# Optimization experiments

Hardware: AMD Instinct MI355X
Metric: run time of the kernel (lower is better)

The kernel has to match this reference:

```python
import jax, jax.numpy as jnp
import numpy as np

BN_EPS = 1e-3  # keras BatchNormalization default epsilon

def _prelu(x, a):
    return jnp.maximum(x, 0) + a * jnp.minimum(x, 0)

def _bn(x, g, b, m, v):
    # inference-mode batchnorm with moving statistics
    return (x - m) * jax.lax.rsqrt(v + BN_EPS) * g + b

def setup_inputs() -> dict:
    key = jax.random.key(0)
    ks = jax.random.split(key, 24)
    B, D, V, L = 4096, 768, 200000, 200000
    F = 3 * D  # 2304 = qid|pos|neg concat
    n = lambda i, shape, s=0.05: jax.random.normal(ks[i], shape, jnp.float32) * s
    return dict(
        qid_embeddings=jax.random.normal(ks[0], (B, D), jnp.float32),
        node_embeddings=n(1, (V, D), 0.1),
        leaf_embeddings=n(2, (L, D), 0.1),
        positives=jax.random.randint(ks[3], (B,), 0, V),
        negetives=jax.random.randint(ks[4], (B,), 0, V),
        p_isleafs=jax.random.randint(ks[5], (B,), 0, 2),
        n_isleafs=jax.random.randint(ks[6], (B,), 0, 2),
        W00=n(7, (F, 36)), b00=jnp.zeros((36,)), a00=jnp.full((36,), 0.25),
        W01=n(8, (36, 1)), b01=jnp.zeros((1,)),
        W1=n(9, (F, 128)), b1=jnp.zeros((128,)), a1=jnp.full((128,), 0.25),
        g1=jnp.ones((128,)), be1=n(10, (128,), 0.1), m1=n(11, (128,), 0.1),
        v1=jax.random.uniform(ks[12], (128,)) + 0.5,
        W2=n(13, (128, 64)), b2=jnp.zeros((64,)), a2=jnp.full((64,), 0.25),
        g2=jnp.ones((64,)), be2=n(14, (64,), 0.1), m2=n(15, (64,), 0.1),
        v2=jax.random.uniform(ks[16], (64,)) + 0.5,
        W3=n(17, (64, 24)), b3=jnp.zeros((24,)), a3=jnp.full((24,), 0.25),
        g3=jnp.ones((24,)), be3=n(18, (24,), 0.1), m3=n(19, (24,), 0.1),
        v3=jax.random.uniform(ks[20], (24,)) + 0.5,
        W4=n(21, (24, 2)), b4=jnp.zeros((2,)),
    )

def reference(qid_embeddings, node_embeddings, leaf_embeddings, positives, negetives,
              p_isleafs, n_isleafs, W00, b00, a00, W01, b01,
              W1, b1, a1, g1, be1, m1, v1,
              W2, b2, a2, g2, be2, m2, v2,
              W3, b3, a3, g3, be3, m3, v3, W4, b4):
    # per-sample conditional embedding gather (leaf table vs internal node table)
    pos = jnp.where((p_isleafs == 1)[:, None], leaf_embeddings[positives], node_embeddings[positives])  # [B,D]
    neg = jnp.where((n_isleafs == 1)[:, None], leaf_embeddings[negetives], node_embeddings[negetives])  # [B,D]
    q = qid_embeddings  # [B,D]
    # attention block: small Dense(36)->Dense(1) scalar weight per sample
    feat = jnp.concatenate([q, pos, neg], axis=1)  # [B,3D]
    h = _prelu(feat @ W00 + b00, a00)              # [B,36]
    w = h @ W01 + b01                              # [B,1]
    item = jnp.concatenate([w * pos, w * neg, q], axis=1)  # [B,3D]
    # MLP 2304 -> 128 -> 64 -> 24 -> 2 (layer10/20/30 unused in original call)
    x = _bn(_prelu(item @ W1 + b1, a1), g1, be1, m1, v1)
    x = _bn(_prelu(x @ W2 + b2, a2), g2, be2, m2, v2)
    x = _bn(_prelu(x @ W3 + b3, a3), g3, be3, m3, v3)
    return jax.nn.softmax(x @ W4 + b4, axis=-1)  # [B,2]
```

## Files before the change

kernel.cpp:

```cpp
#include <hip/hip_runtime.h>
#include <hip/hip_bf16.h>

typedef _Float16 half8 __attribute__((ext_vector_type(8)));
typedef _Float16 half4v __attribute__((ext_vector_type(4)));
typedef float f32x4 __attribute__((ext_vector_type(4)));

#define NCOLS 176
#define TILE_ELEMS (NCOLS*32)
#define TILE_U16 (TILE_ELEMS/8)
#define WTSTR 40
#define XSTR2 2312

#define OFF_A36 0
#define OFF_TQ  2560
#define OFF_TPN 10752
#define OFF_WV  18944
#define OFF_X1  19008
#define OFF_W2  27456
#define OFF_X2  43840
#define OFF_W3  48192
#define OFF_X3  51264
#define OFF_SCR 53056
#define SM_BYTES 77632

struct Params {
  const float *qid, *node, *leaf;
  const int *pos_idx, *neg_idx, *p_leaf, *n_leaf;
  const float *b00, *a00, *W01, *b01;
  const float *b1, *a1, *g1, *be1, *m1, *v1;
  const float *W2, *b2, *a2, *g2, *be2, *m2, *v2;
  const float *W3, *b3, *a3, *g3, *be3, *m3, *v3;
  const float *W4, *b4;
  const _Float16 *Wp;
  float *out;
};

__global__ __launch_bounds__(256) void pack_weights(const float* __restrict__ W00,
                                                    const float* __restrict__ W1,
                                                    _Float16* __restrict__ Wp) {
  int g = blockIdx.x;
  int s = g / 24, t = g - s * 24;
  int k0 = t * 32;
  int w1row0 = (s == 0) ? 1536 : (s == 1 ? 0 : 768);
  __shared__ _Float16 T[NCOLS][WTSTR];
  int tid = threadIdx.x;
  for (int u = tid; u < 1024; u += 256) {
    int kk = u >> 5, c4 = u & 31;
    float4 f = *(const float4*)(W1 + (size_t)(w1row0 + k0 + kk) * 128 + c4 * 4);
    int c = 48 + c4 * 4;
    T[c + 0][kk] = (_Float16)f.x; T[c + 1][kk] = (_Float16)f.y;
    T[c + 2][kk] = (_Float16)f.z; T[c + 3][kk] = (_Float16)f.w;
  }
  for (int u = tid; u < 1152; u += 256) {
    int kk = u / 36, c = u - kk * 36;
    T[c][kk] = (_Float16)W00[(size_t)(s * 768 + k0 + kk) * 36 + c];
  }
  for (int u = tid; u < 384; u += 256) {
    int kk = u & 31, c = 36 + (u >> 5);
    T[c][kk] = (_Float16)0.f;
  }
  __syncthreads();
  uint4* dst = (uint4*)(Wp + (size_t)g * TILE_ELEMS);
  for (int u = tid; u < TILE_U16; u += 256) {
    int c = u >> 2, q = u & 3;
    dst[u] = *(const uint4*)&T[c][q * 8];
  }
}

__global__ __launch_bounds__(512) void fused_main(Params p) {
  __shared__ __align__(16) char sm[SM_BYTES];
  __shared__ const float* Xbase[3][16];

  _Float16* X   = (_Float16*)sm;
  float*    A36 = (float*)(sm + OFF_A36);
  float*    Tq  = (float*)(sm + OFF_TQ);
  float*    Tpn = (float*)(sm + OFF_TPN);
  float*    wv  = (float*)(sm + OFF_WV);
  float*    x1  = (float*)(sm + OFF_X1);
  _Float16* W2h = (_Float16*)(sm + OFF_W2);
  float*    x2  = (float*)(sm + OFF_X2);
  _Float16* W3h = (_Float16*)(sm + OFF_W3);
  float*    x3  = (float*)(sm + OFF_X3);
  float*    scr = (float*)(sm + OFF_SCR);

  const int tid  = threadIdx.x;
  const int wid  = tid >> 6;
  const int lane = tid & 63;
  const int lm   = lane & 15;
  const int hk   = lane >> 4;
  const int nw   = wid & 3;
  const int kg   = wid >> 2;
  const int m0   = blockIdx.x * 16;
  const bool HAS2 = (nw < 3);

  if (tid < 48) {
    int s = tid >> 4, i = tid & 15;
    const float* base;
    if (s == 0) base = p.qid + (size_t)(m0 + i) * 768;
    else if (s == 1) {
      int idx = p.pos_idx[m0 + i];
      base = ((p.p_leaf[m0 + i] == 1) ? p.leaf : p.node) + (size_t)idx * 768;
    } else {
      int idx = p.neg_idx[m0 + i];
      base = ((p.n_leaf[m0 + i] == 1) ? p.leaf : p.node) + (size_t)idx * 768;
    }
    Xbase[s][i] = base;
  }
  __syncthreads();

#pragma unroll
  for (int j = 0; j < 18; ++j) {
    int v = tid + j * 512;
    int i = v / 192, c4 = v - i * 192;
    int s = i >> 4, r = i & 15;
    float4 f = ((const float4*)Xbase[s][i & 15])[c4];
    half4v h = { (_Float16)f.x, (_Float16)f.y, (_Float16)f.z, (_Float16)f.w };
    *(half4v*)(X + r * XSTR2 + s * 768 + c4 * 4) = h;
  }
  __syncthreads();

  const uint4* Wp4 = (const uint4*)p.Wp;
  const int woff = ((nw * 48 + lm) << 2) + hk;

  f32x4 accA[3] = {{0.f,0.f,0.f,0.f},{0.f,0.f,0.f,0.f},{0.f,0.f,0.f,0.f}};
  f32x4 accB[3] = {{0.f,0.f,0.f,0.f},{0.f,0.f,0.f,0.f},{0.f,0.f,0.f,0.f}};

  auto ldW = [&](int g, uint4& r0, uint4& r1, uint4& r2) {
    const uint4* b = Wp4 + (size_t)g * TILE_U16 + woff;
    r0 = b[0]; r1 = b[64];
    if (HAS2) r2 = b[128];
  };
  auto ldA = [&](int g) -> half8 {
    return *(const half8*)(X + lm * XSTR2 + g * 32 + hk * 8);
  };
  auto comp = [&](int g, uint4 w0, uint4 w1, uint4 w2, half8 a) {
    half8 b0 = __builtin_bit_cast(half8, w0);
    half8 b1 = __builtin_bit_cast(half8, w1);
    half8 b2 = __builtin_bit_cast(half8, w2);
    if ((nw == 0) || (g < 24)) {
      accA[0] = __builtin_amdgcn_mfma_f32_16x16x32_f16(a, b0, accA[0], 0, 0, 0);
      accA[1] = __builtin_amdgcn_mfma_f32_16x16x32_f16(a, b1, accA[1], 0, 0, 0);
      if (HAS2) accA[2] = __builtin_amdgcn_mfma_f32_16x16x32_f16(a, b2, accA[2], 0, 0, 0);
    } else {
      accB[0] = __builtin_amdgcn_mfma_f32_16x16x32_f16(a, b0, accB[0], 0, 0, 0);
      accB[1] = __builtin_amdgcn_mfma_f32_16x16x32_f16(a, b1, accB[1], 0, 0, 0);
      if (HAS2) accB[2] = __builtin_amdgcn_mfma_f32_16x16x32_f16(a, b2, accB[2], 0, 0, 0);
    }
  };

  uint4 A0{}, A1{}, A2{}, B0{}, B1{}, B2{};
  half8 aA, aB;
  ldW(kg, A0, A1, A2);     aA = ldA(kg);
  ldW(kg + 2, B0, B1, B2); aB = ldA(kg + 2);
#pragma unroll
  for (int t = 0; t < 36; t += 2) {
    int ga = kg + 2 * t;
    comp(ga, A0, A1, A2, aA);
    if (t + 2 < 36) { ldW(ga + 4, A0, A1, A2); aA = ldA(ga + 4); }
    comp(ga + 2, B0, B1, B2, aB);
    if (t + 3 < 36) { ldW(ga + 6, B0, B1, B2); aB = ldA(ga + 6); }
  }

  __syncthreads();
  if (kg == 1) {
#pragma unroll
    for (int n = 0; n < 3; ++n) {
      if (n < 2 || HAS2) {
#pragma unroll
        for (int r = 0; r < 4; ++r) {
          int base = ((nw * 3 + n) * 2) * 256 + (hk * 4 + r) * 16 + lm;
          scr[base]       = accA[n][r];
          scr[base + 256] = accB[n][r];
        }
      }
    }
  }
  __syncthreads();
  if (kg == 0) {
#pragma unroll
    for (int n = 0; n < 3; ++n) {
      if (n < 2 || HAS2) {
#pragma unroll
        for (int r = 0; r < 4; ++r) {
          int base = ((nw * 3 + n) * 2) * 256 + (hk * 4 + r) * 16 + lm;
          float va = accA[n][r] + scr[base];
          float vb = accB[n][r] + scr[base + 256];
          int row = hk * 4 + r;
          int col = nw * 48 + n * 16 + lm;
          if (nw == 0) { if (col < 36) A36[row * 40 + col] = va; }
          else { int rc = col - 48; Tq[row * 128 + rc] = va; Tpn[row * 128 + rc] = vb; }
        }
      }
    }
  }
  __syncthreads();

#pragma unroll
  for (int j = 0; j < 4; ++j) {
    int u = tid + j * 512;
    float4 f = ((const float4*)p.W2)[u];
    half4v h = { (_Float16)f.x, (_Float16)f.y, (_Float16)f.z, (_Float16)f.w };
    *(half4v*)(W2h + (u >> 4) * 64 + (u & 15) * 4) = h;
  }
  if (tid < 16) {
    float acc = p.b01[0];
    for (int c = 0; c < 36; ++c) {
      float h = A36[tid * 40 + c] + p.b00[c];
      h = (h > 0.f) ? h : p.a00[c] * h;
      acc += h * p.W01[c];
    }
    wv[tid] = acc;
  }
  __syncthreads();

#pragma unroll
  for (int j = 0; j < 4; ++j) {
    int u = tid + j * 512;
    int i = u >> 7, c = u & 127;
    float v = wv[i] * Tpn[i * 128 + c] + Tq[i * 128 + c] + p.b1[c];
    v = (v > 0.f) ? v : p.a1[c] * v;
    v = (v - p.m1[c]) * (1.f / sqrtf(p.v1[c] + 1e-3f)) * p.g1[c] + p.be1[c];
    x1[i * 132 + c] = v;
  }
  __syncthreads();

  if (tid < 256) {
    int i = tid & 15, cq = tid >> 4;
    const float* xr = x1 + i * 132;
    f32x4 acc0 = { p.b2[cq*4+0], p.b2[cq*4+1], p.b2[cq*4+2], p.b2[cq*4+3] };
    f32x4 acc1 = { 0.f, 0.f, 0.f, 0.f };
#pragma unroll 8
    for (int k = 0; k < 128; k += 2) {
      half4v w0 = *(const half4v*)(W2h + k * 64 + cq * 4);
      half4v w1 = *(const half4v*)(W2h + (k + 1) * 64 + cq * 4);
      acc0 += xr[k]     * __builtin_convertvector(w0, f32x4);
      acc1 += xr[k + 1] * __builtin_convertvector(w1, f32x4);
    }
    f32x4 acc = acc0 + acc1;
#pragma unroll
    for (int jj = 0; jj < 4; ++jj) {
      int c = cq * 4 + jj;
      float v = acc[jj];
      v = (v > 0.f) ? v : p.a2[c] * v;
      v = (v - p.m2[c]) * (1.f / sqrtf(p.v2[c] + 1e-3f)) * p.g2[c] + p.be2[c];
      x2[i * 68 + c] = v;
    }
  }
#pragma unroll
  for (int j = 0; j < 3; ++j) {
    int u = tid + j * 512;
    W3h[u] = (_Float16)p.W3[u];
  }
  __syncthreads();

  if (tid < 384) {
    int i = tid & 15, c = tid >> 4;
    float acc = p.b3[c];
#pragma unroll 8
    for (int k = 0; k < 64; ++k) acc += x2[i * 68 + k] * (float)W3h[k * 24 + c];
    acc = (acc > 0.f) ? acc : p.a3[c] * acc;
    acc = (acc - p.m3[c]) * (1.f / sqrtf(p.v3[c] + 1e-3f)) * p.g3[c] + p.be3[c];
    x3[i * 28 + c] = acc;
  }
  __syncthreads();

  if (tid < 16) {
    float l0 = p.b4[0], l1 = p.b4[1];
#pragma unroll
    for (int k = 0; k < 24; ++k) {
      float v = x3[tid * 28 + k];
      l0 += v * p.W4[k * 2 + 0];
      l1 += v * p.W4[k * 2 + 1];
    }
    float m = fmaxf(l0, l1);
    float e0 = __expf(l0 - m), e1 = __expf(l1 - m);
    float inv = 1.f / (e0 + e1);
    p.out[(size_t)(m0 + tid) * 2 + 0] = e0 * inv;
    p.out[(size_t)(m0 + tid) * 2 + 1] = e1 * inv;
  }
}

extern "C" void kernel_launch(void* const* d_in, const int* in_sizes, int n_in,
                              void* d_out, int out_size, void* d_ws, size_t ws_size,
                              hipStream_t stream) {
  const float* qid  = (const float*)d_in[0];
  const float* node = (const float*)d_in[1];
  const float* leaf = (const float*)d_in[2];
  const int* positives = (const int*)d_in[3];
  const int* negetives = (const int*)d_in[4];
  const int* p_isleafs = (const int*)d_in[5];
  const int* n_isleafs = (const int*)d_in[6];
  const float* W00 = (const float*)d_in[7];
  const float* b00 = (const float*)d_in[8];
  const float* a00 = (const float*)d_in[9];
  const float* W01 = (const float*)d_in[10];
  const float* b01 = (const float*)d_in[11];
  const float* W1  = (const float*)d_in[12];
  const float* b1  = (const float*)d_in[13];
  const float* a1  = (const float*)d_in[14];
  const float* g1  = (const float*)d_in[15];
  const float* be1 = (const float*)d_in[16];
  const float* m1  = (const float*)d_in[17];
  const float* v1  = (const float*)d_in[18];
  const float* W2  = (const float*)d_in[19];
  const float* b2  = (const float*)d_in[20];
  const float* a2  = (const float*)d_in[21];
  const float* g2  = (const float*)d_in[22];
  const float* be2 = (const float*)d_in[23];
  const float* m2  = (const float*)d_in[24];
  const float* v2  = (const float*)d_in[25];
  const float* W3  = (const float*)d_in[26];
  const float* b3  = (const float*)d_in[27];
  const float* a3  = (const float*)d_in[28];
  const float* g3  = (const float*)d_in[29];
  const float* be3 = (const float*)d_in[30];
  const float* m3  = (const float*)d_in[31];
  const float* v3  = (const float*)d_in[32];
  const float* W4  = (const float*)d_in[33];
  const float* b4  = (const float*)d_in[34];

  _Float16* Wp = (_Float16*)d_ws;

  pack_weights<<<72, 256, 0, stream>>>(W00, W1, Wp);

  Params p;
  p.qid = qid; p.node = node; p.leaf = leaf;
  p.pos_idx = positives; p.neg_idx = negetives; p.p_leaf = p_isleafs; p.n_leaf = n_isleafs;
  p.b00 = b00; p.a00 = a00; p.W01 = W01; p.b01 = b01;
  p.b1 = b1; p.a1 = a1; p.g1 = g1; p.be1 = be1; p.m1 = m1; p.v1 = v1;
  p.W2 = W2; p.b2 = b2; p.a2 = a2; p.g2 = g2; p.be2 = be2; p.m2 = m2; p.v2 = v2;
  p.W3 = W3; p.b3 = b3; p.a3 = a3; p.g3 = g3; p.be3 = be3; p.m3 = m3; p.v3 = v3;
  p.W4 = W4; p.b4 = b4;
  p.Wp = Wp;
  p.out = (float*)d_out;

  int B = in_sizes[3];
  fused_main<<<B / 16, 512, 0, stream>>>(p);
}
```

Before: 41.41 us.

## Halve rows per block to 8 and deepen weight prefetch to three stages

Each block now handles 8 samples instead of 16, doubling the grid to 512 blocks and shrinking shared memory so more blocks can be resident (launch bounds request 4 blocks per CU). The MFMA 16-row tile is kept, with rows 8-15 duplicating rows 0-7, so half the MFMA work is wasted. Weight fragments for the first three k-groups are issued before the gather to overlap latency, and the main loop now rotates three register buffers instead of two. The packed weight stream is re-read by twice as many blocks, which raises L2 traffic in exchange for better latency hiding.

```diff
diff --git a/kernel.cpp b/kernel.cpp
--- a/kernel.cpp
+++ b/kernel.cpp
@@ -10,18 +10,19 @@
 #define TILE_U16 (TILE_ELEMS/8)
 #define WTSTR 40
 #define XSTR2 2312
+#define BM 8
 
 #define OFF_A36 0
-#define OFF_TQ  2560
-#define OFF_TPN 10752
-#define OFF_WV  18944
-#define OFF_X1  19008
-#define OFF_W2  27456
-#define OFF_X2  43840
-#define OFF_W3  48192
-#define OFF_X3  51264
-#define OFF_SCR 53056
-#define SM_BYTES 77632
+#define OFF_TQ  1280
+#define OFF_TPN 5376
+#define OFF_WV  9472
+#define OFF_X1  9536
+#define OFF_W2  13760
+#define OFF_X2  30144
+#define OFF_W3  32320
+#define OFF_X3  35392
+#define OFF_SCR 37184
+#define SM_BYTES 49472
 
 struct Params {
   const float *qid, *node, *leaf;
@@ -67,9 +68,9 @@
   }
 }
 
-__global__ __launch_bounds__(512) void fused_main(Params p) {
+__global__ __launch_bounds__(512, 4) void fused_main(Params p) {
   __shared__ __align__(16) char sm[SM_BYTES];
-  __shared__ const float* Xbase[3][16];
+  __shared__ const float* Xbase[3][BM];
 
   _Float16* X   = (_Float16*)sm;
   float*    A36 = (float*)(sm + OFF_A36);
@@ -87,14 +88,28 @@
   const int wid  = tid >> 6;
   const int lane = tid & 63;
   const int lm   = lane & 15;
+  const int rowA = lm & 7;
   const int hk   = lane >> 4;
   const int nw   = wid & 3;
   const int kg   = wid >> 2;
-  const int m0   = blockIdx.x * 16;
+  const int m0   = blockIdx.x * BM;
   const bool HAS2 = (nw < 3);
 
-  if (tid < 48) {
-    int s = tid >> 4, i = tid & 15;
+  const uint4* Wp4 = (const uint4*)p.Wp;
+  const int woff = ((nw * 48 + lm) << 2) + hk;
+  uint4 A0{}, A1{}, A2{}, B0{}, B1{}, B2{}, C0{}, C1{}, C2{};
+  {
+    const uint4* b0 = Wp4 + (size_t)kg * TILE_U16 + woff;
+    const uint4* b1 = Wp4 + (size_t)(kg + 2) * TILE_U16 + woff;
+    const uint4* b2 = Wp4 + (size_t)(kg + 4) * TILE_U16 + woff;
+    A0 = b0[0]; A1 = b0[64];
+    B0 = b1[0]; B1 = b1[64];
+    C0 = b2[0]; C1 = b2[64];
+    if (HAS2) { A2 = b0[128]; B2 = b1[128]; C2 = b2[128]; }
+  }
+
+  if (tid < 3 * BM) {
+    int s = tid >> 3, i = tid & 7;
     const float* base;
     if (s == 0) base = p.qid + (size_t)(m0 + i) * 768;
     else if (s == 1) {
@@ -109,18 +124,15 @@
   __syncthreads();
 
 #pragma unroll
-  for (int j = 0; j < 18; ++j) {
+  for (int j = 0; j < 9; ++j) {
     int v = tid + j * 512;
     int i = v / 192, c4 = v - i * 192;
-    int s = i >> 4, r = i & 15;
-    float4 f = ((const float4*)Xbase[s][i & 15])[c4];
+    int s = i >> 3, r = i & 7;
+    float4 f = ((const float4*)Xbase[s][r])[c4];
     half4v h = { (_Float16)f.x, (_Float16)f.y, (_Float16)f.z, (_Float16)f.w };
     *(half4v*)(X + r * XSTR2 + s * 768 + c4 * 4) = h;
   }
   __syncthreads();
-
-  const uint4* Wp4 = (const uint4*)p.Wp;
-  const int woff = ((nw * 48 + lm) << 2) + hk;
 
   f32x4 accA[3] = {{0.f,0.f,0.f,0.f},{0.f,0.f,0.f,0.f},{0.f,0.f,0.f,0.f}};
   f32x4 accB[3] = {{0.f,0.f,0.f,0.f},{0.f,0.f,0.f,0.f},{0.f,0.f,0.f,0.f}};
@@ -131,7 +143,7 @@
     if (HAS2) r2 = b[128];
   };
   auto ldA = [&](int g) -> half8 {
-    return *(const half8*)(X + lm * XSTR2 + g * 32 + hk * 8);
+    return *(const half8*)(X + rowA * XSTR2 + g * 32 + hk * 8);
   };
   auto comp = [&](int g, uint4 w0, uint4 w1, uint4 w2, half8 a) {
     half8 b0 = __builtin_bit_cast(half8, w0);
@@ -148,43 +160,41 @@
     }
   };
 
-  uint4 A0{}, A1{}, A2{}, B0{}, B1{}, B2{};
-  half8 aA, aB;
-  ldW(kg, A0, A1, A2);     aA = ldA(kg);
-  ldW(kg + 2, B0, B1, B2); aB = ldA(kg + 2);
-#pragma unroll
-  for (int t = 0; t < 36; t += 2) {
-    int ga = kg + 2 * t;
-    comp(ga, A0, A1, A2, aA);
-    if (t + 2 < 36) { ldW(ga + 4, A0, A1, A2); aA = ldA(ga + 4); }
-    comp(ga + 2, B0, B1, B2, aB);
-    if (t + 3 < 36) { ldW(ga + 6, B0, B1, B2); aB = ldA(ga + 6); }
-  }
-
-  __syncthreads();
-  if (kg == 1) {
+  half8 aA = ldA(kg), aB = ldA(kg + 2), aC = ldA(kg + 4);
+#pragma unroll
+  for (int t = 0; t < 36; t += 3) {
+    int g = kg + 2 * t;
+    comp(g, A0, A1, A2, aA);
+    if (t + 3 < 36) { ldW(g + 6, A0, A1, A2); aA = ldA(g + 6); }
+    comp(g + 2, B0, B1, B2, aB);
+    if (t + 4 < 36) { ldW(g + 8, B0, B1, B2); aB = ldA(g + 8); }
+    comp(g + 4, C0, C1, C2, aC);
+    if (t + 5 < 36) { ldW(g + 10, C0, C1, C2); aC = ldA(g + 10); }
+  }
+
+  if (kg == 1 && hk < 2) {
 #pragma unroll
     for (int n = 0; n < 3; ++n) {
       if (n < 2 || HAS2) {
 #pragma unroll
         for (int r = 0; r < 4; ++r) {
-          int base = ((nw * 3 + n) * 2) * 256 + (hk * 4 + r) * 16 + lm;
+          int base = ((nw * 3 + n) * 2) * 128 + (hk * 4 + r) * 16 + lm;
           scr[base]       = accA[n][r];
-          scr[base + 256] = accB[n][r];
+          scr[base + 128] = accB[n][r];
         }
       }
     }
   }
   __syncthreads();
-  if (kg == 0) {
+  if (kg == 0 && hk < 2) {
 #pragma unroll
     for (int n = 0; n < 3; ++n) {
       if (n < 2 || HAS2) {
 #pragma unroll
         for (int r = 0; r < 4; ++r) {
-          int base = ((nw * 3 + n) * 2) * 256 + (hk * 4 + r) * 16 + lm;
+          int base = ((nw * 3 + n) * 2) * 128 + (hk * 4 + r) * 16 + lm;
           float va = accA[n][r] + scr[base];
-          float vb = accB[n][r] + scr[base + 256];
+          float vb = accB[n][r] + scr[base + 128];
           int row = hk * 4 + r;
           int col = nw * 48 + n * 16 + lm;
           if (nw == 0) { if (col < 36) A36[row * 40 + col] = va; }
@@ -202,7 +212,7 @@
     half4v h = { (_Float16)f.x, (_Float16)f.y, (_Float16)f.z, (_Float16)f.w };
     *(half4v*)(W2h + (u >> 4) * 64 + (u & 15) * 4) = h;
   }
-  if (tid < 16) {
+  if (tid < BM) {
     float acc = p.b01[0];
     for (int c = 0; c < 36; ++c) {
       float h = A36[tid * 40 + c] + p.b00[c];
@@ -214,7 +224,7 @@
   __syncthreads();
 
 #pragma unroll
-  for (int j = 0; j < 4; ++j) {
+  for (int j = 0; j < 2; ++j) {
     int u = tid + j * 512;
     int i = u >> 7, c = u & 127;
     float v = wv[i] * Tpn[i * 128 + c] + Tq[i * 128 + c] + p.b1[c];
@@ -224,8 +234,8 @@
   }
   __syncthreads();
 
-  if (tid < 256) {
-    int i = tid & 15, cq = tid >> 4;
+  if (tid < 16 * BM) {
+    int i = tid & 7, cq = tid >> 3;
     const float* xr = x1 + i * 132;
     f32x4 acc0 = { p.b2[cq*4+0], p.b2[cq*4+1], p.b2[cq*4+2], p.b2[cq*4+3] };
     f32x4 acc1 = { 0.f, 0.f, 0.f, 0.f };
@@ -246,15 +256,14 @@
       x2[i * 68 + c] = v;
     }
   }
-#pragma unroll
   for (int j = 0; j < 3; ++j) {
     int u = tid + j * 512;
     W3h[u] = (_Float16)p.W3[u];
   }
   __syncthreads();
 
-  if (tid < 384) {
-    int i = tid & 15, c = tid >> 4;
+  if (tid < 24 * BM) {
+    int i = tid & 7, c = tid >> 3;
     float acc = p.b3[c];
 #pragma unroll 8
     for (int k = 0; k < 64; ++k) acc += x2[i * 68 + k] * (float)W3h[k * 24 + c];
@@ -264,7 +273,7 @@
   }
   __syncthreads();
 
-  if (tid < 16) {
+  if (tid < BM) {
     float l0 = p.b4[0], l1 = p.b4[1];
 #pragma unroll
     for (int k = 0; k < 24; ++k) {
@@ -307,8 +316,8 @@
   const float* a2  = (const float*)d_in[21];
   const float* g2  = (const float*)d_in[22];
   const float* be2 = (const float*)d_in[23];
+  const float* v2  = (const float*)d_in[25];
   const float* m2  = (const float*)d_in[24];
-  const float* v2  = (const float*)d_in[25];
   const float* W3  = (const float*)d_in[26];
   const float* b3  = (const float*)d_in[27];
   const float* a3  = (const float*)d_in[28];
@@ -335,5 +344,5 @@
   p.out = (float*)d_out;
 
   int B = in_sizes[3];
-  fused_main<<<B / 16, 512, 0, stream>>>(p);
+  fused_main<<<B / BM, 512, 0, stream>>>(p);
 }
```

After: 47.54 us. +14.8%, slower.

## Pipeline embedding gather stages with MFMA K-loop and prefetch weights early

Applied to the files above, without the earlier changes.

Splits the qid/pos/neg staging into three segments loaded into registers and written to shared memory one segment ahead, so MFMA work on one segment overlaps the global gathers of the next. Weight tiles are now prefetched four deep into a register ring, starting before the gather setup. W2 is also loaded during the last segment instead of after the GEMM. The cost is higher register pressure from the staging and weight buffers, which may reduce occupancy or cause spills at 512 threads.

```diff
diff --git a/kernel.cpp b/kernel.cpp
--- a/kernel.cpp
+++ b/kernel.cpp
@@ -10,6 +10,7 @@
 #define TILE_U16 (TILE_ELEMS/8)
 #define WTSTR 40
 #define XSTR2 2312
+#define BM 16
 
 #define OFF_A36 0
 #define OFF_TQ  2560
@@ -69,7 +70,7 @@
 
 __global__ __launch_bounds__(512) void fused_main(Params p) {
   __shared__ __align__(16) char sm[SM_BYTES];
-  __shared__ const float* Xbase[3][16];
+  __shared__ const float* Xbase[3][BM];
 
   _Float16* X   = (_Float16*)sm;
   float*    A36 = (float*)(sm + OFF_A36);
@@ -90,10 +91,24 @@
   const int hk   = lane >> 4;
   const int nw   = wid & 3;
   const int kg   = wid >> 2;
-  const int m0   = blockIdx.x * 16;
+  const int m0   = blockIdx.x * BM;
   const bool HAS2 = (nw < 3);
 
-  if (tid < 48) {
+  const uint4* Wp4 = (const uint4*)p.Wp;
+  const int woff = ((nw * 48 + lm) << 2) + hk;
+
+  uint4 P[4][3];
+  auto ldWp = [&](int j) {
+    int s = j / 12;
+    int g = s * 24 + kg + 2 * (j - s * 12);
+    const uint4* b = Wp4 + (size_t)g * TILE_U16 + woff;
+    P[j & 3][0] = b[0]; P[j & 3][1] = b[64];
+    if (HAS2) P[j & 3][2] = b[128];
+  };
+
+  ldWp(0); ldWp(1); ldWp(2); ldWp(3);
+
+  if (tid < 3 * BM) {
     int s = tid >> 4, i = tid & 15;
     const float* base;
     if (s == 0) base = p.qid + (size_t)(m0 + i) * 768;
@@ -106,37 +121,45 @@
     }
     Xbase[s][i] = base;
   }
-  __syncthreads();
-
-#pragma unroll
-  for (int j = 0; j < 18; ++j) {
-    int v = tid + j * 512;
-    int i = v / 192, c4 = v - i * 192;
-    int s = i >> 4, r = i & 15;
-    float4 f = ((const float4*)Xbase[s][i & 15])[c4];
-    half4v h = { (_Float16)f.x, (_Float16)f.y, (_Float16)f.z, (_Float16)f.w };
-    *(half4v*)(X + r * XSTR2 + s * 768 + c4 * 4) = h;
-  }
-  __syncthreads();
-
-  const uint4* Wp4 = (const uint4*)p.Wp;
-  const int woff = ((nw * 48 + lm) << 2) + hk;
+
+  float4 sregA[6], sregB[6];
+  auto stageLoad = [&](int s, float4* sr) {
+#pragma unroll
+    for (int jj = 0; jj < 6; ++jj) {
+      int v = tid + jj * 512;
+      int i = v / 192, c4 = v - i * 192;
+      const float* b = (s == 0) ? (p.qid + (size_t)(m0 + i) * 768) : Xbase[s][i];
+      sr[jj] = ((const float4*)b)[c4];
+    }
+  };
+  auto stageWrite = [&](int s, const float4* sr) {
+#pragma unroll
+    for (int jj = 0; jj < 6; ++jj) {
+      int v = tid + jj * 512;
+      int i = v / 192, c4 = v - i * 192;
+      float4 f = sr[jj];
+      half4v h = { (_Float16)f.x, (_Float16)f.y, (_Float16)f.z, (_Float16)f.w };
+      *(half4v*)(X + i * XSTR2 + s * 768 + c4 * 4) = h;
+    }
+  };
+
+  stageLoad(0, sregA);
+  __syncthreads();
+  stageLoad(1, sregB);
+  stageWrite(0, sregA);
+  __syncthreads();
 
   f32x4 accA[3] = {{0.f,0.f,0.f,0.f},{0.f,0.f,0.f,0.f},{0.f,0.f,0.f,0.f}};
   f32x4 accB[3] = {{0.f,0.f,0.f,0.f},{0.f,0.f,0.f,0.f},{0.f,0.f,0.f,0.f}};
-
-  auto ldW = [&](int g, uint4& r0, uint4& r1, uint4& r2) {
-    const uint4* b = Wp4 + (size_t)g * TILE_U16 + woff;
-    r0 = b[0]; r1 = b[64];
-    if (HAS2) r2 = b[128];
-  };
+  half8 av[3];
+
   auto ldA = [&](int g) -> half8 {
     return *(const half8*)(X + lm * XSTR2 + g * 32 + hk * 8);
   };
-  auto comp = [&](int g, uint4 w0, uint4 w1, uint4 w2, half8 a) {
-    half8 b0 = __builtin_bit_cast(half8, w0);
-    half8 b1 = __builtin_bit_cast(half8, w1);
-    half8 b2 = __builtin_bit_cast(half8, w2);
+  auto comp = [&](int g, int slot, half8 a) {
+    half8 b0 = __builtin_bit_cast(half8, P[slot][0]);
+    half8 b1 = __builtin_bit_cast(half8, P[slot][1]);
+    half8 b2 = __builtin_bit_cast(half8, P[slot][2]);
     if ((nw == 0) || (g < 24)) {
       accA[0] = __builtin_amdgcn_mfma_f32_16x16x32_f16(a, b0, accA[0], 0, 0, 0);
       accA[1] = __builtin_amdgcn_mfma_f32_16x16x32_f16(a, b1, accA[1], 0, 0, 0);
@@ -148,17 +171,29 @@
     }
   };
 
-  uint4 A0{}, A1{}, A2{}, B0{}, B1{}, B2{};
-  half8 aA, aB;
-  ldW(kg, A0, A1, A2);     aA = ldA(kg);
-  ldW(kg + 2, B0, B1, B2); aB = ldA(kg + 2);
-#pragma unroll
-  for (int t = 0; t < 36; t += 2) {
-    int ga = kg + 2 * t;
-    comp(ga, A0, A1, A2, aA);
-    if (t + 2 < 36) { ldW(ga + 4, A0, A1, A2); aA = ldA(ga + 4); }
-    comp(ga + 2, B0, B1, B2, aB);
-    if (t + 3 < 36) { ldW(ga + 6, B0, B1, B2); aB = ldA(ga + 6); }
+  float4 w2r[4];
+#pragma unroll
+  for (int s = 0; s < 3; ++s) {
+    if (s == 1) {
+      stageLoad(2, sregA);
+      stageWrite(1, sregB);
+      __syncthreads();
+    }
+    if (s == 2) {
+#pragma unroll
+      for (int jj = 0; jj < 4; ++jj) w2r[jj] = ((const float4*)p.W2)[tid + jj * 512];
+      stageWrite(2, sregA);
+      __syncthreads();
+    }
+    const int gb = s * 24 + kg;
+    av[0] = ldA(gb); av[1] = ldA(gb + 2); av[2] = ldA(gb + 4);
+#pragma unroll
+    for (int tt = 0; tt < 12; ++tt) {
+      int j = s * 12 + tt;
+      comp(gb + 2 * tt, j & 3, av[tt % 3]);
+      if (j + 4 < 36) ldWp(j + 4);
+      if (tt + 3 < 12) av[tt % 3] = ldA(gb + 2 * (tt + 3));
+    }
   }
 
   __syncthreads();
@@ -196,13 +231,13 @@
   __syncthreads();
 
 #pragma unroll
-  for (int j = 0; j < 4; ++j) {
-    int u = tid + j * 512;
-    float4 f = ((const float4*)p.W2)[u];
+  for (int jj = 0; jj < 4; ++jj) {
+    int u = tid + jj * 512;
+    float4 f = w2r[jj];
     half4v h = { (_Float16)f.x, (_Float16)f.y, (_Float16)f.z, (_Float16)f.w };
     *(half4v*)(W2h + (u >> 4) * 64 + (u & 15) * 4) = h;
   }
-  if (tid < 16) {
+  if (tid < BM) {
     float acc = p.b01[0];
     for (int c = 0; c < 36; ++c) {
       float h = A36[tid * 40 + c] + p.b00[c];
@@ -246,7 +281,6 @@
       x2[i * 68 + c] = v;
     }
   }
-#pragma unroll
   for (int j = 0; j < 3; ++j) {
     int u = tid + j * 512;
     W3h[u] = (_Float16)p.W3[u];
@@ -264,7 +298,7 @@
   }
   __syncthreads();
 
-  if (tid < 16) {
+  if (tid < BM) {
     float l0 = p.b4[0], l1 = p.b4[1];
 #pragma unroll
     for (int k = 0; k < 24; ++k) {
@@ -335,5 +369,5 @@
   p.out = (float*)d_out;
 
   int B = in_sizes[3];
-  fused_main<<<B / 16, 512, 0, stream>>>(p);
+  fused_main<<<B / BM, 512, 0, stream>>>(p);
 }
```

Result: faster. 38.51 us (-7.0%).

## Move embedding gather into prep kernel and stream A operand from global

Applied to the files above, without the earlier changes.

The pos/neg embedding gather and fp16 conversion move into the weight-packing prep kernel, which writes a compact fp16 [B,1536] buffer to workspace. The main kernel then drops its LDS staging of X and loads A fragments straight from global memory, converting qid rows from fp32 on the fly, with a deeper 4-stage weight prefetch and 6-deep A prefetch. W2 is also prefetched into registers before the reduction. The cost is an extra global round trip for the gathered rows in exchange for removing the LDS staging, its barriers and the gather latency from the main kernel.

```diff
diff --git a/kernel.cpp b/kernel.cpp
--- a/kernel.cpp
+++ b/kernel.cpp
@@ -9,7 +9,8 @@
 #define TILE_ELEMS (NCOLS*32)
 #define TILE_U16 (TILE_ELEMS/8)
 #define WTSTR 40
-#define XSTR2 2312
+#define BM 16
+#define XPN_OFF (1u<<20)
 
 #define OFF_A36 0
 #define OFF_TQ  2560
@@ -26,52 +27,70 @@
 struct Params {
   const float *qid, *node, *leaf;
   const int *pos_idx, *neg_idx, *p_leaf, *n_leaf;
+  const float *W00, *W1;
   const float *b00, *a00, *W01, *b01;
   const float *b1, *a1, *g1, *be1, *m1, *v1;
   const float *W2, *b2, *a2, *g2, *be2, *m2, *v2;
   const float *W3, *b3, *a3, *g3, *be3, *m3, *v3;
   const float *W4, *b4;
-  const _Float16 *Wp;
+  _Float16 *Wp;
+  _Float16 *Xpn;
   float *out;
 };
 
-__global__ __launch_bounds__(256) void pack_weights(const float* __restrict__ W00,
-                                                    const float* __restrict__ W1,
-                                                    _Float16* __restrict__ Wp) {
-  int g = blockIdx.x;
-  int s = g / 24, t = g - s * 24;
-  int k0 = t * 32;
-  int w1row0 = (s == 0) ? 1536 : (s == 1 ? 0 : 768);
-  __shared__ _Float16 T[NCOLS][WTSTR];
-  int tid = threadIdx.x;
-  for (int u = tid; u < 1024; u += 256) {
-    int kk = u >> 5, c4 = u & 31;
-    float4 f = *(const float4*)(W1 + (size_t)(w1row0 + k0 + kk) * 128 + c4 * 4);
-    int c = 48 + c4 * 4;
-    T[c + 0][kk] = (_Float16)f.x; T[c + 1][kk] = (_Float16)f.y;
-    T[c + 2][kk] = (_Float16)f.z; T[c + 3][kk] = (_Float16)f.w;
-  }
-  for (int u = tid; u < 1152; u += 256) {
-    int kk = u / 36, c = u - kk * 36;
-    T[c][kk] = (_Float16)W00[(size_t)(s * 768 + k0 + kk) * 36 + c];
-  }
-  for (int u = tid; u < 384; u += 256) {
-    int kk = u & 31, c = 36 + (u >> 5);
-    T[c][kk] = (_Float16)0.f;
-  }
-  __syncthreads();
-  uint4* dst = (uint4*)(Wp + (size_t)g * TILE_ELEMS);
-  for (int u = tid; u < TILE_U16; u += 256) {
-    int c = u >> 2, q = u & 3;
-    dst[u] = *(const uint4*)&T[c][q * 8];
+__global__ __launch_bounds__(256) void prep(Params p) {
+  const int b = blockIdx.x;
+  const int tid = threadIdx.x;
+  if (b < 72) {
+    int g = b;
+    int s = g / 24, t = g - s * 24;
+    int k0 = t * 32;
+    int w1row0 = (s == 0) ? 1536 : (s == 1 ? 0 : 768);
+    __shared__ _Float16 T[NCOLS][WTSTR];
+    for (int u = tid; u < 1024; u += 256) {
+      int kk = u >> 5, c4 = u & 31;
+      float4 f = *(const float4*)(p.W1 + (size_t)(w1row0 + k0 + kk) * 128 + c4 * 4);
+      int c = 48 + c4 * 4;
+      T[c + 0][kk] = (_Float16)f.x; T[c + 1][kk] = (_Float16)f.y;
+      T[c + 2][kk] = (_Float16)f.z; T[c + 3][kk] = (_Float16)f.w;
+    }
+    for (int u = tid; u < 1152; u += 256) {
+      int kk = u / 36, c = u - kk * 36;
+      T[c][kk] = (_Float16)p.W00[(size_t)(s * 768 + k0 + kk) * 36 + c];
+    }
+    for (int u = tid; u < 384; u += 256) {
+      int kk = u & 31, c = 36 + (u >> 5);
+      T[c][kk] = (_Float16)0.f;
+    }
+    __syncthreads();
+    uint4* dst = (uint4*)(p.Wp + (size_t)g * TILE_ELEMS);
+    for (int u = tid; u < TILE_U16; u += 256) {
+      int c = u >> 2, q = u & 3;
+      dst[u] = *(const uint4*)&T[c][q * 8];
+    }
+  } else {
+    int gb = b - 72;
+#pragma unroll
+    for (int j = 0; j < 3; ++j) {
+      int id = gb * 256 + tid + j * 262144;
+      int s  = id / 192;
+      int r  = id - s * 192;
+      int seg = r / 96;
+      int c4  = r - seg * 96;
+      int idx = (seg == 0 ? p.pos_idx : p.neg_idx)[s];
+      int lf  = (seg == 0 ? p.p_leaf  : p.n_leaf )[s];
+      const float* src = ((lf == 1) ? p.leaf : p.node) + (size_t)idx * 768 + c4 * 8;
+      float4 fa = *(const float4*)src;
+      float4 fb = *(const float4*)(src + 4);
+      half8 h = { (_Float16)fa.x, (_Float16)fa.y, (_Float16)fa.z, (_Float16)fa.w,
+                  (_Float16)fb.x, (_Float16)fb.y, (_Float16)fb.z, (_Float16)fb.w };
+      *(half8*)(p.Xpn + (size_t)s * 1536 + seg * 768 + c4 * 8) = h;
+    }
   }
 }
 
-__global__ __launch_bounds__(512) void fused_main(Params p) {
+__global__ __launch_bounds__(512) void gemm_tail(Params p) {
   __shared__ __align__(16) char sm[SM_BYTES];
-  __shared__ const float* Xbase[3][16];
-
-  _Float16* X   = (_Float16*)sm;
   float*    A36 = (float*)(sm + OFF_A36);
   float*    Tq  = (float*)(sm + OFF_TQ);
   float*    Tpn = (float*)(sm + OFF_TPN);
@@ -90,54 +109,45 @@
   const int hk   = lane >> 4;
   const int nw   = wid & 3;
   const int kg   = wid >> 2;
-  const int m0   = blockIdx.x * 16;
+  const int m0   = blockIdx.x * BM;
   const bool HAS2 = (nw < 3);
 
-  if (tid < 48) {
-    int s = tid >> 4, i = tid & 15;
-    const float* base;
-    if (s == 0) base = p.qid + (size_t)(m0 + i) * 768;
-    else if (s == 1) {
-      int idx = p.pos_idx[m0 + i];
-      base = ((p.p_leaf[m0 + i] == 1) ? p.leaf : p.node) + (size_t)idx * 768;
-    } else {
-      int idx = p.neg_idx[m0 + i];
-      base = ((p.n_leaf[m0 + i] == 1) ? p.leaf : p.node) + (size_t)idx * 768;
-    }
-    Xbase[s][i] = base;
-  }
-  __syncthreads();
-
-#pragma unroll
-  for (int j = 0; j < 18; ++j) {
-    int v = tid + j * 512;
-    int i = v / 192, c4 = v - i * 192;
-    int s = i >> 4, r = i & 15;
-    float4 f = ((const float4*)Xbase[s][i & 15])[c4];
-    half4v h = { (_Float16)f.x, (_Float16)f.y, (_Float16)f.z, (_Float16)f.w };
-    *(half4v*)(X + r * XSTR2 + s * 768 + c4 * 4) = h;
-  }
-  __syncthreads();
+  const float*     qrow = p.qid + (size_t)(m0 + lm) * 768;
+  const _Float16*  xrow = p.Xpn + (size_t)(m0 + lm) * 1536;
 
   const uint4* Wp4 = (const uint4*)p.Wp;
   const int woff = ((nw * 48 + lm) << 2) + hk;
 
+  uint4 P[4][3];
+  auto ldWp = [&](int t) {
+    const uint4* b = Wp4 + (size_t)(kg + 2 * t) * TILE_U16 + woff;
+    P[t & 3][0] = b[0]; P[t & 3][1] = b[64];
+    if (HAS2) P[t & 3][2] = b[128];
+  };
+
+  half8 av[6];
+#define LDA(t) ( (t) < 12 ? ({ \
+      const float* s_ = qrow + (kg + 2*(t)) * 32 + hk * 8; \
+      float4 fa_ = *(const float4*)s_; \
+      float4 fb_ = *(const float4*)(s_ + 4); \
+      half8 h_ = { (_Float16)fa_.x, (_Float16)fa_.y, (_Float16)fa_.z, (_Float16)fa_.w, \
+                   (_Float16)fb_.x, (_Float16)fb_.y, (_Float16)fb_.z, (_Float16)fb_.w }; h_; }) \
+    : *(const half8*)(xrow + (kg + 2*(t) - 24) * 32 + hk * 8) )
+
   f32x4 accA[3] = {{0.f,0.f,0.f,0.f},{0.f,0.f,0.f,0.f},{0.f,0.f,0.f,0.f}};
   f32x4 accB[3] = {{0.f,0.f,0.f,0.f},{0.f,0.f,0.f,0.f},{0.f,0.f,0.f,0.f}};
 
-  auto ldW = [&](int g, uint4& r0, uint4& r1, uint4& r2) {
-    const uint4* b = Wp4 + (size_t)g * TILE_U16 + woff;
-    r0 = b[0]; r1 = b[64];
-    if (HAS2) r2 = b[128];
-  };
-  auto ldA = [&](int g) -> half8 {
-    return *(const half8*)(X + lm * XSTR2 + g * 32 + hk * 8);
-  };
-  auto comp = [&](int g, uint4 w0, uint4 w1, uint4 w2, half8 a) {
-    half8 b0 = __builtin_bit_cast(half8, w0);
-    half8 b1 = __builtin_bit_cast(half8, w1);
-    half8 b2 = __builtin_bit_cast(half8, w2);
-    if ((nw == 0) || (g < 24)) {
+  ldWp(0); ldWp(1); ldWp(2); ldWp(3);
+  av[0] = LDA(0); av[1] = LDA(1); av[2] = LDA(2);
+  av[3] = LDA(3); av[4] = LDA(4); av[5] = LDA(5);
+
+#pragma unroll
+  for (int t = 0; t < 36; ++t) {
+    half8 a  = av[t % 6];
+    half8 b0 = __builtin_bit_cast(half8, P[t & 3][0]);
+    half8 b1 = __builtin_bit_cast(half8, P[t & 3][1]);
+    half8 b2 = __builtin_bit_cast(half8, P[t & 3][2]);
+    if ((nw == 0) || (t < 12)) {
       accA[0] = __builtin_amdgcn_mfma_f32_16x16x32_f16(a, b0, accA[0], 0, 0, 0);
       accA[1] = __builtin_amdgcn_mfma_f32_16x16x32_f16(a, b1, accA[1], 0, 0, 0);
       if (HAS2) accA[2] = __builtin_amdgcn_mfma_f32_16x16x32_f16(a, b2, accA[2], 0, 0, 0);
@@ -146,22 +156,14 @@
       accB[1] = __builtin_amdgcn_mfma_f32_16x16x32_f16(a, b1, accB[1], 0, 0, 0);
       if (HAS2) accB[2] = __builtin_amdgcn_mfma_f32_16x16x32_f16(a, b2, accB[2], 0, 0, 0);
     }
-  };
-
-  uint4 A0{}, A1{}, A2{}, B0{}, B1{}, B2{};
-  half8 aA, aB;
-  ldW(kg, A0, A1, A2);     aA = ldA(kg);
-  ldW(kg + 2, B0, B1, B2); aB = ldA(kg + 2);
-#pragma unroll
-  for (int t = 0; t < 36; t += 2) {
-    int ga = kg + 2 * t;
-    comp(ga, A0, A1, A2, aA);
-    if (t + 2 < 36) { ldW(ga + 4, A0, A1, A2); aA = ldA(ga + 4); }
-    comp(ga + 2, B0, B1, B2, aB);
-    if (t + 3 < 36) { ldW(ga + 6, B0, B1, B2); aB = ldA(ga + 6); }
-  }
-
-  __syncthreads();
+    if (t + 4 < 36) ldWp(t + 4);
+    if (t + 6 < 36) av[t % 6] = LDA(t + 6);
+  }
+
+  float4 w2r[4];
+#pragma unroll
+  for (int jj = 0; jj < 4; ++jj) w2r[jj] = ((const float4*)p.W2)[tid + jj * 512];
+
   if (kg == 1) {
 #pragma unroll
     for (int n = 0; n < 3; ++n) {
@@ -196,13 +198,13 @@
   __syncthreads();
 
 #pragma unroll
-  for (int j = 0; j < 4; ++j) {
-    int u = tid + j * 512;
-    float4 f = ((const float4*)p.W2)[u];
+  for (int jj = 0; jj < 4; ++jj) {
+    int u = tid + jj * 512;
+    float4 f = w2r[jj];
     half4v h = { (_Float16)f.x, (_Float16)f.y, (_Float16)f.z, (_Float16)f.w };
     *(half4v*)(W2h + (u >> 4) * 64 + (u & 15) * 4) = h;
   }
-  if (tid < 16) {
+  if (tid < BM) {
     float acc = p.b01[0];
     for (int c = 0; c < 36; ++c) {
       float h = A36[tid * 40 + c] + p.b00[c];
@@ -246,10 +248,9 @@
       x2[i * 68 + c] = v;
     }
   }
-#pragma unroll
   for (int j = 0; j < 3; ++j) {
     int u = tid + j * 512;
-    W3h[u] = (_Float16)p.W3[u];
+    if (u < 1536) W3h[u] = (_Float16)p.W3[u];
   }
   __syncthreads();
 
@@ -264,7 +265,7 @@
   }
   __syncthreads();
 
-  if (tid < 16) {
+  if (tid < BM) {
     float l0 = p.b4[0], l1 = p.b4[1];
 #pragma unroll
     for (int k = 0; k < 24; ++k) {
@@ -283,57 +284,47 @@
 extern "C" void kernel_launch(void* const* d_in, const int* in_sizes, int n_in,
                               void* d_out, int out_size, void* d_ws, size_t ws_size,
                               hipStream_t stream) {
-  const float* qid  = (const float*)d_in[0];
-  const float* node = (const float*)d_in[1];
-  const float* leaf = (const float*)d_in[2];
-  const int* positives = (const int*)d_in[3];
-  const int* negetives = (const int*)d_in[4];
-  const int* p_isleafs = (const int*)d_in[5];
-  const int* n_isleafs = (const int*)d_in[6];
-  const float* W00 = (const float*)d_in[7];
-  const float* b00 = (const float*)d_in[8];
-  const float* a00 = (const float*)d_in[9];
-  const float* W01 = (const float*)d_in[10];
-  const float* b01 = (const float*)d_in[11];
-  const float* W1  = (const float*)d_in[12];
-  const float* b1  = (const float*)d_in[13];
-  const float* a1  = (const float*)d_in[14];
-  const float* g1  = (const float*)d_in[15];
-  const float* be1 = (const float*)d_in[16];
-  const float* m1  = (const float*)d_in[17];
-  const float* v1  = (const float*)d_in[18];
-  const float* W2  = (const float*)d_in[19];
-  const float* b2  = (const float*)d_in[20];
-  const float* a2  = (const float*)d_in[21];
-  const float* g2  = (const float*)d_in[22];
-  const float* be2 = (const float*)d_in[23];
-  const float* m2  = (const float*)d_in[24];
-  const float* v2  = (const float*)d_in[25];
-  const float* W3  = (const float*)d_in[26];
-  const float* b3  = (const float*)d_in[27];
-  const float* a3  = (const float*)d_in[28];
-  const float* g3  = (const float*)d_in[29];
-  const float* be3 = (const float*)d_in[30];
-  const float* m3  = (const float*)d_in[31];
-  const float* v3  = (const float*)d_in[32];
-  const float* W4  = (const float*)d_in[33];
-  const float* b4  = (const float*)d_in[34];
-
-  _Float16* Wp = (_Float16*)d_ws;
-
-  pack_weights<<<72, 256, 0, stream>>>(W00, W1, Wp);
-
   Params p;
-  p.qid = qid; p.node = node; p.leaf = leaf;
-  p.pos_idx = positives; p.neg_idx = negetives; p.p_leaf = p_isleafs; p.n_leaf = n_isleafs;
-  p.b00 = b00; p.a00 = a00; p.W01 = W01; p.b01 = b01;
-  p.b1 = b1; p.a1 = a1; p.g1 = g1; p.be1 = be1; p.m1 = m1; p.v1 = v1;
-  p.W2 = W2; p.b2 = b2; p.a2 = a2; p.g2 = g2; p.be2 = be2; p.m2 = m2; p.v2 = v2;
-  p.W3 = W3; p.b3 = b3; p.a3 = a3; p.g3 = g3; p.be3 = be3; p.m3 = m3; p.v3 = v3;
-  p.W4 = W4; p.b4 = b4;
-  p.Wp = Wp;
+  p.qid  = (const float*)d_in[0];
+  p.node = (const float*)d_in[1];
+  p.leaf = (const float*)d_in[2];
+  p.pos_idx = (const int*)d_in[3];
+  p.neg_idx = (const int*)d_in[4];
+  p.p_leaf  = (const int*)d_in[5];
+  p.n_leaf  = (const int*)d_in[6];
+  p.W00 = (const float*)d_in[7];
+  p.b00 = (const float*)d_in[8];
+  p.a00 = (const float*)d_in[9];
+  p.W01 = (const float*)d_in[10];
+  p.b01 = (const float*)d_in[11];
+  p.W1  = (const float*)d_in[12];
+  p.b1  = (const float*)d_in[13];
+  p.a1  = (const float*)d_in[14];
+  p.g1  = (const float*)d_in[15];
+  p.be1 = (const float*)d_in[16];
+  p.m1  = (const float*)d_in[17];
+  p.v1  = (const float*)d_in[18];
+  p.W2  = (const float*)d_in[19];
+  p.b2  = (const float*)d_in[20];
+  p.a2  = (const float*)d_in[21];
+  p.g2  = (const float*)d_in[22];
+  p.be2 = (const float*)d_in[23];
+  p.m2  = (const float*)d_in[24];
+  p.v2  = (const float*)d_in[25];
+  p.W3  = (const float*)d_in[26];
+  p.b3  = (const float*)d_in[27];
+  p.a3  = (const float*)d_in[28];
+  p.g3  = (const float*)d_in[29];
+  p.be3 = (const float*)d_in[30];
+  p.m3  = (const float*)d_in[31];
+  p.v3  = (const float*)d_in[32];
+  p.W4  = (const float*)d_in[33];
+  p.b4  = (const float*)d_in[34];
+  p.Wp  = (_Float16*)d_ws;
+  p.Xpn = (_Float16*)((char*)d_ws + XPN_OFF);
   p.out = (float*)d_out;
 
+  prep<<<1096, 256, 0, stream>>>(p);
   int B = in_sizes[3];
-  fused_main<<<B / 16, 512, 0, stream>>>(p);
+  gemm_tail<<<B / BM, 512, 0, stream>>>(p);
 }
```

Result: slower. 49.39 us (+19.3%).
